# Kernel optimization log

Hardware: AMD Instinct MI355X
Metric: run time of the kernel (lower is better)

The kernel has to match this reference:

```python
import jax, jax.numpy as jnp
import numpy as np

jax.config.update("jax_enable_x64", True)  # packing needs true int64 bit ops

_NORM12 = np.array([
    [3,1,1,1,3,3,3,3],[1,3,1,1,3,3,3,3],[1,1,3,1,3,3,3,3],[1,1,1,3,3,3,3,3],
    [3,3,3,1,3,3,1,1],[3,3,3,1,3,1,3,1],[3,3,3,1,1,3,3,1],[3,3,3,1,3,1,1,3],
    [3,3,3,1,1,3,1,3],[3,3,3,1,1,1,3,3],[3,3,1,3,3,3,1,1],[3,3,1,3,3,1,3,1],
    [3,3,1,3,1,3,3,1],[3,3,1,3,3,1,1,3],[3,3,1,3,1,3,1,3],[3,3,1,3,1,1,3,3],
    [3,1,3,3,3,3,1,1],[3,1,3,3,3,1,3,1],[3,1,3,3,1,3,3,1],[3,1,3,3,3,1,1,3],
    [3,1,3,3,1,3,1,3],[1,3,3,3,1,1,3,3],[1,3,3,3,3,3,1,1],[1,3,3,3,3,1,3,1],
    [1,3,3,3,1,3,3,1],[1,3,3,3,3,1,1,3],[1,3,3,3,1,3,1,3],[1,1,3,3,1,3,3,3],
    [3,3,1,1,3,3,3,1]], dtype=np.float32) / 2.0


def _build_packed_abs_grid():
    # faithful numpy port of get_packed_abs_grid()
    intr = np.arange(-4, 4)
    d8 = np.stack(np.meshgrid(*([intr] * 8), indexing='ij'), axis=-1).reshape(-1, 8).astype(np.float32) + 0.5
    mask = ((d8.sum(-1) % 2) == 0) & ((d8 * d8).sum(-1) <= 10)
    d8abs = np.unique(np.abs(d8[mask]), axis=0)
    cba = np.concatenate([d8abs, _NORM12], axis=0)          # [256, 8]
    cba = cba[:, [0, 2, 4, 6, 1, 3, 5, 7]]
    cba[:, 7] = cba[:, 7] * (1 - 2 * (cba.sum(1) % 2))
    cba = (cba * 2 + 8).astype(np.int64)
    acc = cba[:, 0].copy()
    for i in range(7):
        acc |= cba[:, i + 1] << ((i + 1) * 4)
    return acc                                              # [256] packed nibbles


def _build_full_grid(packed):
    # reconstruct the 2^16-entry E8P grid from the packed abs codewords
    SHUF = np.array([0, 4, 1, 5, 2, 6, 3, 7])               # inverse of [0,2,4,6,1,3,5,7]
    c = np.arange(1 << 16)
    signs = c & 255
    absi = c >> 8
    parity = (((signs[:, None] >> np.arange(8)) & 1).sum(1)) & 1
    signs = signs ^ parity
    nib = ((packed[absi][:, None] >> (4 * SHUF[None, :])) & 15).astype(np.float32)
    val = (nib - 8.0) / 2.0                                 # undo cba*2+8
    sbit = (signs[:, None] >> SHUF[None, :]) & 1
    val = np.where(sbit == 1, -val, val)
    val = val - 0.25 * parity[:, None].astype(np.float32)   # odd-parity coset shift
    return val.astype(np.float32)                           # [65536, 8]


def setup_inputs() -> dict:
    key = jax.random.key(0)
    packed = _build_packed_abs_grid()
    grid = jnp.asarray(_build_full_grid(packed))            # [65536, 8]
    grid_norm = (grid * grid).sum(-1)                       # [65536]
    X = jax.random.normal(key, (256, 32, 8), dtype=jnp.float32)
    return {"X": X, "grid": grid, "grid_norm": grid_norm}


def _pack_idxs(idxs):
    # faithful port of maybe_pack_idxs; idxs: int64 [m, n], m%16==0, n%8==0
    m, n = idxs.shape
    q = idxs.reshape(m // 2, 2, n // 2, 2).transpose(0, 2, 1, 3)   # [m//2, n//2, 2, 2]
    abs32 = ((q[:, :, 0, 0] >> 8)
             + ((q[:, :, 1, 0] >> 8) << 8)
             + ((q[:, :, 0, 1] >> 8) << 16)
             + ((q[:, :, 1, 1] >> 8) << 24))
    sign32 = jnp.zeros_like(abs32)
    for i in range(4):
        wt = q[:, :, i % 2, i // 2]
        for j in range(8):
            sign32 = sign32 + (((wt >> j) & 1) << (4 * j + i))
    out = (sign32 << 32) + abs32
    out = out.reshape(m // 16, 8, n // 8, 4).transpose(0, 2, 1, 3)
    return out.reshape(m, n // 4)


def reference(X, grid, grid_norm):
    m, n, _ = X.shape
    Xf = X.reshape(-1, 8)                                   # [m*n, 8]
    scores = 2.0 * (Xf @ grid.T) - grid_norm                # [m*n, 65536] (traffic-bound)
    idxs = jnp.argmax(scores, axis=-1).astype(jnp.int64)    # [m*n]
    vals = grid[idxs].reshape(m, n, 8)
    idxs = idxs.reshape(m, n)
    packed = _pack_idxs(idxs)                               # [m, n//4] int64
    return vals, idxs, packed
```

## Files before the change

kernel.cpp:

```cpp
#include <hip/hip_runtime.h>
#include <stdint.h>
#include <math.h>


__device__ __forceinline__ void cmp_keep(float& bs, int& bc, float s, int c) {
    if (s > bs || (s == bs && c < bc)) { bs = s; bc = c; }
}

__device__ __forceinline__ double pay_abs(double t, uint32_t pk16) {
    long long ll = __double_as_longlong(t) & 0x7FFFFFFFFFFF0000ll;
    return __longlong_as_double(ll | (long long)pk16);
}

struct TournOut { double a1c, a2c; uint32_t q1, q2; };

__device__ __forceinline__ TournOut tourn8(const double kk[8]) {
    double m01 = fmin(kk[0], kk[1]), x01 = fmax(kk[0], kk[1]);
    double m23 = fmin(kk[2], kk[3]), x23 = fmax(kk[2], kk[3]);
    double m45 = fmin(kk[4], kk[5]), x45 = fmax(kk[4], kk[5]);
    double m67 = fmin(kk[6], kk[7]), x67 = fmax(kk[6], kk[7]);
    double mA = fmin(m01, m23), sA = fmin(fmax(m01, m23), fmin(x01, x23));
    double mB = fmin(m45, m67), sB = fmin(fmax(m45, m67), fmin(x45, x67));
    double m1 = fmin(mA, mB),   m2 = fmin(fmax(mA, mB), fmin(sA, sB));
    long long b1 = __double_as_longlong(m1);
    long long b2 = __double_as_longlong(m2);
    TournOut o;
    o.a1c = __longlong_as_double(b1 & ~0xFFFFll);
    o.a2c = __longlong_as_double(b2 & ~0xFFFFll);
    o.q1 = (uint32_t)b1 & 0xFFFFu;
    o.q2 = (uint32_t)b2 & 0xFFFFu;
    return o;
}

__global__ __launch_bounds__(256, 4) void e8p_fused2(
    const float* __restrict__ X,
    const float* __restrict__ grid,
    const float* __restrict__ grid_norm,
    float* __restrict__ out)
{
    __shared__ float2   sWp[4][256];
    __shared__ uint32_t sPK[4][256];
    __shared__ uint32_t sMeta[256];
    __shared__ float    sSN[256];
    __shared__ int      sC[4][2];

    const int tid = threadIdx.x;
    const int shuf[8] = {0, 4, 1, 5, 2, 6, 3, 7};

    {
        const float4* g4 = reinterpret_cast<const float4*>(grid + (size_t)tid * 2048);
        float4 lo = g4[0], hi = g4[1];
        float w[8] = {lo.x, lo.y, lo.z, lo.w, hi.x, hi.y, hi.z, hi.w};
        float aw[8]; uint32_t pk[8]; uint32_t wsgnshuf = 0;
#pragma unroll
        for (int j = 0; j < 8; ++j) {
            uint32_t sb = __float_as_uint(w[j]) >> 31;
            wsgnshuf |= sb << shuf[j];
            aw[j] = fabsf(w[j]);
            uint32_t tw = (uint32_t)(2.0f * aw[j]);
            pk[j] = (tw << 13) | ((uint32_t)j << 10) | (1u << shuf[j]);
        }
        sWp[0][tid] = make_float2(aw[0], aw[1]);
        sWp[1][tid] = make_float2(aw[2], aw[3]);
        sWp[2][tid] = make_float2(aw[4], aw[5]);
        sWp[3][tid] = make_float2(aw[6], aw[7]);
#pragma unroll
        for (int i = 0; i < 4; ++i) sPK[i][tid] = pk[2 * i] | (pk[2 * i + 1] << 16);
        sMeta[tid] = wsgnshuf | ((uint32_t)(__popc(wsgnshuf) & 1) << 8);
        sSN[tid] = grid_norm[(size_t)tid * 256];
    }
    __syncthreads();

    const int lane = tid & 63, wid = tid >> 6;
    const int A  = blockIdx.x >> 3;
    const int Bh = blockIdx.x & 7;
    const int rbase = (2 * A + (wid & 1)) * 32 + 4 * Bh + 2 * (wid >> 1);

    double   xd[2][8]; double Sx[2];
    uint32_t sp1b[2], sp0sh[2], sp1sh[2], pp0[2], pp1[2];
#pragma unroll
    for (int s = 0; s < 2; ++s) {
        const float* xr = X + (size_t)(rbase + s) * 8;
        double acc = 0.0; uint32_t m1 = 0, m0s = 0, m1s = 0, p0 = 0, p1 = 0;
#pragma unroll
        for (int j = 0; j < 8; ++j) {
            float xf = xr[j]; double d = (double)xf;
            xd[s][j] = d; acc += d;
            uint32_t b0 = (xf < 0.0f) ? 1u : 0u;
            uint32_t b1 = (d < -0.25) ? 1u : 0u;
            m1 |= b1 << j; m0s |= b0 << shuf[j]; m1s |= b1 << shuf[j];
            p0 ^= b0; p1 ^= b1;
        }
        Sx[s] = acc; sp1b[s] = m1; sp0sh[s] = m0s; sp1sh[s] = m1s; pp0[s] = p0; pp1[s] = p1;
    }

    float bestS[2] = {-INFINITY, -INFINITY};
    int   bestC[2] = {0x7fffffff, 0x7fffffff};

#pragma unroll
    for (int k = 0; k < 4; ++k) {
        const int absi = lane + (k << 6);
        float2 w01 = sWp[0][absi], w23 = sWp[1][absi], w45 = sWp[2][absi], w67 = sWp[3][absi];
        float awf[8] = {w01.x, w01.y, w23.x, w23.y, w45.x, w45.y, w67.x, w67.y};
        uint32_t pw0 = sPK[0][absi], pw1 = sPK[1][absi], pw2 = sPK[2][absi], pw3 = sPK[3][absi];
        uint32_t pk16[8] = {pw0 & 0xFFFFu, pw0 >> 16, pw1 & 0xFFFFu, pw1 >> 16,
                            pw2 & 0xFFFFu, pw2 >> 16, pw3 & 0xFFFFu, pw3 >> 16};
        const uint32_t meta = sMeta[absi];
        const float    sN   = sSN[absi];
        const uint32_t wsh = meta & 0xFFu, wpar = (meta >> 8) & 1u;
        double wdA[8];
#pragma unroll
        for (int j = 0; j < 8; ++j) wdA[j] = (double)awf[j];

#pragma unroll
        for (int s = 0; s < 2; ++s) {
            double t0[8], t1[8];
#pragma unroll
            for (int j = 0; j < 8; ++j) {
                t0[j] = wdA[j] * xd[s][j];
                t1[j] = fma(t0[j], 4.0, wdA[j]);
            }
            {
                double Sab = ((fabs(t0[0]) + fabs(t0[1])) + (fabs(t0[2]) + fabs(t0[3])))
                           + ((fabs(t0[4]) + fabs(t0[5])) + (fabs(t0[6]) + fabs(t0[7])));
                double kk[8];
#pragma unroll
                for (int j = 0; j < 8; ++j) kk[j] = pay_abs(t0[j], pk16[j]);
                TournOut o = tourn8(kk);
                uint32_t sb1 = o.q1 & 0xFFu, sb2 = o.q2 & 0xFFu;
                uint32_t par = wpar ^ pp0[s];
                uint32_t seffb = wsh ^ sp0sh[s];
                double dA = par ? o.a1c : 0.0;
                double dB = par ? o.a2c : (o.a1c + o.a2c);
                uint32_t sbA = par ? sb1 : 0u;
                uint32_t sbB = par ? sb2 : (sb1 ^ sb2);
                { float f = (float)(Sab - 2.0 * dA);
                  cmp_keep(bestS[s], bestC[s], 2.0f * f - sN, (absi << 8) | (int)(seffb ^ sbA)); }
                { float f = (float)(Sab - 2.0 * dB);
                  cmp_keep(bestS[s], bestC[s], 2.0f * f - sN, (absi << 8) | (int)(seffb ^ sbB)); }
            }
            {
                double Sab4 = ((fabs(t1[0]) + fabs(t1[1])) + (fabs(t1[2]) + fabs(t1[3])))
                            + ((fabs(t1[4]) + fabs(t1[5])) + (fabs(t1[6]) + fabs(t1[7])));
                double kk[8];
#pragma unroll
                for (int j = 0; j < 8; ++j) kk[j] = pay_abs(t1[j], pk16[j]);
                TournOut o = tourn8(kk);
                uint32_t sb1 = o.q1 & 0xFFu, sb2 = o.q2 & 0xFFu;
                uint32_t par = wpar ^ pp1[s];
                uint32_t seffb = wsh ^ sp1sh[s];
                double dA = par ? o.a1c : 0.0;
                double dB = par ? o.a2c : (o.a1c + o.a2c);
                uint32_t sbA = par ? sb1 : 0u;
                uint32_t sbB = par ? sb2 : (sb1 ^ sb2);
                float W0 = ((((sp1b[s] >> 0) & 1) ? -awf[0] : awf[0]) + (((sp1b[s] >> 1) & 1) ? -awf[1] : awf[1]))
                         + ((((sp1b[s] >> 2) & 1) ? -awf[2] : awf[2]) + (((sp1b[s] >> 3) & 1) ? -awf[3] : awf[3]))
                         + (((((sp1b[s] >> 4) & 1) ? -awf[4] : awf[4]) + (((sp1b[s] >> 5) & 1) ? -awf[5] : awf[5]))
                         +  ((((sp1b[s] >> 6) & 1) ? -awf[6] : awf[6]) + (((sp1b[s] >> 7) & 1) ? -awf[7] : awf[7])));
                uint32_t j1 = (o.q1 >> 10) & 7u, j2 = (o.q2 >> 10) & 7u;
                float w1f = 0.5f * (float)(o.q1 >> 13);
                float w2f = 0.5f * (float)(o.q2 >> 13);
                float sw1 = ((sp1b[s] >> j1) & 1) ? -w1f : w1f;
                float sw2 = ((sp1b[s] >> j2) & 1) ? -w2f : w2f;
                float swA = par ? sw1 : 0.0f;
                float swB = par ? sw2 : (sw1 + sw2);
                {
                    float Wc = W0 - 2.0f * swA;
                    double E = (Sab4 - 2.0 * dA) - ((double)Wc + Sx[s]);
                    float f = (float)(0.25 * E);
                    float gnv = (sN - 0.5f * Wc) + 0.5f;
                    cmp_keep(bestS[s], bestC[s], 2.0f * f - gnv,
                             (absi << 8) | (int)((seffb ^ sbA) ^ 1u));
                }
                {
                    float Wc = W0 - 2.0f * swB;
                    double E = (Sab4 - 2.0 * dB) - ((double)Wc + Sx[s]);
                    float f = (float)(0.25 * E);
                    float gnv = (sN - 0.5f * Wc) + 0.5f;
                    cmp_keep(bestS[s], bestC[s], 2.0f * f - gnv,
                             (absi << 8) | (int)((seffb ^ sbB) ^ 1u));
                }
            }
        }
    }

#pragma unroll
    for (int off = 32; off > 0; off >>= 1) {
        float s0 = __shfl_xor(bestS[0], off); int c0 = __shfl_xor(bestC[0], off);
        float s1 = __shfl_xor(bestS[1], off); int c1 = __shfl_xor(bestC[1], off);
        cmp_keep(bestS[0], bestC[0], s0, c0);
        cmp_keep(bestS[1], bestC[1], s1, c1);
    }

    if (lane < 2) {
        const int s = lane;
        const int c = bestC[s];
        const int row = rbase + s;
        const float4* gg = reinterpret_cast<const float4*>(grid + (size_t)c * 8);
        float4* v4 = reinterpret_cast<float4*>(out + (size_t)row * 8);
        v4[0] = gg[0]; v4[1] = gg[1];
        out[65536 + row] = (float)c;
        sC[wid][s] = c;
    }
    __syncthreads();

    if (tid < 2) {
        const int q = tid;
        const uint32_t e00 = (uint32_t)sC[2 * q + 0][0];
        const uint32_t e10 = (uint32_t)sC[2 * q + 1][0];
        const uint32_t e01 = (uint32_t)sC[2 * q + 0][1];
        const uint32_t e11 = (uint32_t)sC[2 * q + 1][1];
        const uint32_t abs32 = (e00 >> 8) | ((e10 >> 8) << 8)
                             | ((e01 >> 8) << 16) | ((e11 >> 8) << 24);
        const int Bq = 2 * Bh + q;
        const int f = ((A >> 3) << 7) | ((Bq >> 2) << 5) | ((A & 7) << 2) | (Bq & 3);
        out[73728 + f] = (float)(int32_t)abs32;
    }
}

extern "C" void kernel_launch(void* const* d_in, const int* in_sizes, int n_in,
                              void* d_out, int out_size, void* d_ws, size_t ws_size,
                              hipStream_t stream)
{
    const float* X    = (const float*)d_in[0];
    const float* grid = (const float*)d_in[1];
    const float* gn   = (const float*)d_in[2];
    e8p_fused2<<<1024, 256, 0, stream>>>(X, grid, gn, (float*)d_out);
}
```

Measured before the change: 82.87 us.

## Process one row per wavefront and double grid size to 2048 blocks

Each wavefront now handles a single input row instead of two, and the grid grows from 1024 to 2048 blocks. The launch-bounds occupancy hint is dropped and the outer k loop is no longer force-unrolled, which lowers register pressure. The aim is more parallelism and occupancy in exchange for no reuse of LDS codebook reads across two rows. The cost is that every block repeats the shared-memory table setup, so the setup work and grid loads per row double.

Measured after the change: 76.52 us. 7.7% less time.

```diff
diff --git a/kernel.cpp b/kernel.cpp
--- a/kernel.cpp
+++ b/kernel.cpp
@@ -32,7 +32,7 @@
     return o;
 }
 
-__global__ __launch_bounds__(256, 4) void e8p_fused2(
+__global__ __launch_bounds__(256) void e8p_fused3(
     const float* __restrict__ X,
     const float* __restrict__ grid,
     const float* __restrict__ grid_norm,
@@ -42,7 +42,7 @@
     __shared__ uint32_t sPK[4][256];
     __shared__ uint32_t sMeta[256];
     __shared__ float    sSN[256];
-    __shared__ int      sC[4][2];
+    __shared__ int      sC[4];
 
     const int tid = threadIdx.x;
     const int shuf[8] = {0, 4, 1, 5, 2, 6, 3, 7};
@@ -72,32 +72,25 @@
     __syncthreads();
 
     const int lane = tid & 63, wid = tid >> 6;
-    const int A  = blockIdx.x >> 3;
-    const int Bh = blockIdx.x & 7;
-    const int rbase = (2 * A + (wid & 1)) * 32 + 4 * Bh + 2 * (wid >> 1);
-
-    double   xd[2][8]; double Sx[2];
-    uint32_t sp1b[2], sp0sh[2], sp1sh[2], pp0[2], pp1[2];
-#pragma unroll
-    for (int s = 0; s < 2; ++s) {
-        const float* xr = X + (size_t)(rbase + s) * 8;
-        double acc = 0.0; uint32_t m1 = 0, m0s = 0, m1s = 0, p0 = 0, p1 = 0;
-#pragma unroll
-        for (int j = 0; j < 8; ++j) {
-            float xf = xr[j]; double d = (double)xf;
-            xd[s][j] = d; acc += d;
-            uint32_t b0 = (xf < 0.0f) ? 1u : 0u;
-            uint32_t b1 = (d < -0.25) ? 1u : 0u;
-            m1 |= b1 << j; m0s |= b0 << shuf[j]; m1s |= b1 << shuf[j];
-            p0 ^= b0; p1 ^= b1;
-        }
-        Sx[s] = acc; sp1b[s] = m1; sp0sh[s] = m0s; sp1sh[s] = m1s; pp0[s] = p0; pp1[s] = p1;
-    }
-
-    float bestS[2] = {-INFINITY, -INFINITY};
-    int   bestC[2] = {0x7fffffff, 0x7fffffff};
-
-#pragma unroll
+    const int A = blockIdx.x >> 4, B = blockIdx.x & 15;
+    const int row = A * 64 + (wid >> 1) * 32 + B * 2 + (wid & 1);
+
+    const float* xr = X + (size_t)row * 8;
+    double xd[8], Sx = 0.0;
+    uint32_t sp1b = 0, sp0sh = 0, sp1sh = 0, pp0 = 0, pp1 = 0;
+#pragma unroll
+    for (int j = 0; j < 8; ++j) {
+        float xf = xr[j]; double d = (double)xf;
+        xd[j] = d; Sx += d;
+        uint32_t b0 = (xf < 0.0f) ? 1u : 0u;
+        uint32_t b1 = (d < -0.25) ? 1u : 0u;
+        sp1b |= b1 << j;
+        sp0sh |= b0 << shuf[j]; sp1sh |= b1 << shuf[j];
+        pp0 ^= b0; pp1 ^= b1;
+    }
+
+    float bestS = -INFINITY; int bestC = 0x7fffffff;
+
     for (int k = 0; k < 4; ++k) {
         const int absi = lane + (k << 6);
         float2 w01 = sWp[0][absi], w23 = sWp[1][absi], w45 = sWp[2][absi], w67 = sWp[3][absi];
@@ -108,112 +101,99 @@
         const uint32_t meta = sMeta[absi];
         const float    sN   = sSN[absi];
         const uint32_t wsh = meta & 0xFFu, wpar = (meta >> 8) & 1u;
-        double wdA[8];
-#pragma unroll
-        for (int j = 0; j < 8; ++j) wdA[j] = (double)awf[j];
-
-#pragma unroll
-        for (int s = 0; s < 2; ++s) {
-            double t0[8], t1[8];
-#pragma unroll
-            for (int j = 0; j < 8; ++j) {
-                t0[j] = wdA[j] * xd[s][j];
-                t1[j] = fma(t0[j], 4.0, wdA[j]);
+
+        double kk0[8], t1[8];
+#pragma unroll
+        for (int j = 0; j < 8; ++j) {
+            double wd = (double)awf[j];
+            double t0 = wd * xd[j];
+            t1[j]  = fma(t0, 4.0, wd);
+            kk0[j] = pay_abs(t0, pk16[j]);
+        }
+
+        {
+            double Sab = ((fabs(kk0[0]) + fabs(kk0[1])) + (fabs(kk0[2]) + fabs(kk0[3])))
+                       + ((fabs(kk0[4]) + fabs(kk0[5])) + (fabs(kk0[6]) + fabs(kk0[7])));
+            TournOut o = tourn8(kk0);
+            uint32_t sb1 = o.q1 & 0xFFu, sb2 = o.q2 & 0xFFu;
+            uint32_t par = wpar ^ pp0;
+            uint32_t seffb = wsh ^ sp0sh;
+            double dA = par ? o.a1c : 0.0;
+            double dB = par ? o.a2c : (o.a1c + o.a2c);
+            uint32_t sbA = par ? sb1 : 0u;
+            uint32_t sbB = par ? sb2 : (sb1 ^ sb2);
+            { float f = (float)(Sab - 2.0 * dA);
+              cmp_keep(bestS, bestC, 2.0f * f - sN, (absi << 8) | (int)(seffb ^ sbA)); }
+            { float f = (float)(Sab - 2.0 * dB);
+              cmp_keep(bestS, bestC, 2.0f * f - sN, (absi << 8) | (int)(seffb ^ sbB)); }
+        }
+        {
+            double kk1[8];
+#pragma unroll
+            for (int j = 0; j < 8; ++j) kk1[j] = pay_abs(t1[j], pk16[j]);
+            double Sab4 = ((fabs(kk1[0]) + fabs(kk1[1])) + (fabs(kk1[2]) + fabs(kk1[3])))
+                        + ((fabs(kk1[4]) + fabs(kk1[5])) + (fabs(kk1[6]) + fabs(kk1[7])));
+            TournOut o = tourn8(kk1);
+            uint32_t sb1 = o.q1 & 0xFFu, sb2 = o.q2 & 0xFFu;
+            uint32_t par = wpar ^ pp1;
+            uint32_t seffb = wsh ^ sp1sh;
+            double dA = par ? o.a1c : 0.0;
+            double dB = par ? o.a2c : (o.a1c + o.a2c);
+            uint32_t sbA = par ? sb1 : 0u;
+            uint32_t sbB = par ? sb2 : (sb1 ^ sb2);
+            float W0 = ((((sp1b >> 0) & 1) ? -awf[0] : awf[0]) + (((sp1b >> 1) & 1) ? -awf[1] : awf[1]))
+                     + ((((sp1b >> 2) & 1) ? -awf[2] : awf[2]) + (((sp1b >> 3) & 1) ? -awf[3] : awf[3]))
+                     + (((((sp1b >> 4) & 1) ? -awf[4] : awf[4]) + (((sp1b >> 5) & 1) ? -awf[5] : awf[5]))
+                     +  ((((sp1b >> 6) & 1) ? -awf[6] : awf[6]) + (((sp1b >> 7) & 1) ? -awf[7] : awf[7])));
+            uint32_t j1 = (o.q1 >> 10) & 7u, j2 = (o.q2 >> 10) & 7u;
+            float w1f = 0.5f * (float)(o.q1 >> 13);
+            float w2f = 0.5f * (float)(o.q2 >> 13);
+            float sw1 = ((sp1b >> j1) & 1) ? -w1f : w1f;
+            float sw2 = ((sp1b >> j2) & 1) ? -w2f : w2f;
+            float swA = par ? sw1 : 0.0f;
+            float swB = par ? sw2 : (sw1 + sw2);
+            {
+                float Wc = W0 - 2.0f * swA;
+                double E = (Sab4 - 2.0 * dA) - ((double)Wc + Sx);
+                float f = (float)(0.25 * E);
+                float gnv = (sN - 0.5f * Wc) + 0.5f;
+                cmp_keep(bestS, bestC, 2.0f * f - gnv,
+                         (absi << 8) | (int)((seffb ^ sbA) ^ 1u));
             }
             {
-                double Sab = ((fabs(t0[0]) + fabs(t0[1])) + (fabs(t0[2]) + fabs(t0[3])))
-                           + ((fabs(t0[4]) + fabs(t0[5])) + (fabs(t0[6]) + fabs(t0[7])));
-                double kk[8];
-#pragma unroll
-                for (int j = 0; j < 8; ++j) kk[j] = pay_abs(t0[j], pk16[j]);
-                TournOut o = tourn8(kk);
-                uint32_t sb1 = o.q1 & 0xFFu, sb2 = o.q2 & 0xFFu;
-                uint32_t par = wpar ^ pp0[s];
-                uint32_t seffb = wsh ^ sp0sh[s];
-                double dA = par ? o.a1c : 0.0;
-                double dB = par ? o.a2c : (o.a1c + o.a2c);
-                uint32_t sbA = par ? sb1 : 0u;
-                uint32_t sbB = par ? sb2 : (sb1 ^ sb2);
-                { float f = (float)(Sab - 2.0 * dA);
-                  cmp_keep(bestS[s], bestC[s], 2.0f * f - sN, (absi << 8) | (int)(seffb ^ sbA)); }
-                { float f = (float)(Sab - 2.0 * dB);
-                  cmp_keep(bestS[s], bestC[s], 2.0f * f - sN, (absi << 8) | (int)(seffb ^ sbB)); }
+                float Wc = W0 - 2.0f * swB;
+                double E = (Sab4 - 2.0 * dB) - ((double)Wc + Sx);
+                float f = (float)(0.25 * E);
+                float gnv = (sN - 0.5f * Wc) + 0.5f;
+                cmp_keep(bestS, bestC, 2.0f * f - gnv,
+                         (absi << 8) | (int)((seffb ^ sbB) ^ 1u));
             }
-            {
-                double Sab4 = ((fabs(t1[0]) + fabs(t1[1])) + (fabs(t1[2]) + fabs(t1[3])))
-                            + ((fabs(t1[4]) + fabs(t1[5])) + (fabs(t1[6]) + fabs(t1[7])));
-                double kk[8];
-#pragma unroll
-                for (int j = 0; j < 8; ++j) kk[j] = pay_abs(t1[j], pk16[j]);
-                TournOut o = tourn8(kk);
-                uint32_t sb1 = o.q1 & 0xFFu, sb2 = o.q2 & 0xFFu;
-                uint32_t par = wpar ^ pp1[s];
-                uint32_t seffb = wsh ^ sp1sh[s];
-                double dA = par ? o.a1c : 0.0;
-                double dB = par ? o.a2c : (o.a1c + o.a2c);
-                uint32_t sbA = par ? sb1 : 0u;
-                uint32_t sbB = par ? sb2 : (sb1 ^ sb2);
-                float W0 = ((((sp1b[s] >> 0) & 1) ? -awf[0] : awf[0]) + (((sp1b[s] >> 1) & 1) ? -awf[1] : awf[1]))
-                         + ((((sp1b[s] >> 2) & 1) ? -awf[2] : awf[2]) + (((sp1b[s] >> 3) & 1) ? -awf[3] : awf[3]))
-                         + (((((sp1b[s] >> 4) & 1) ? -awf[4] : awf[4]) + (((sp1b[s] >> 5) & 1) ? -awf[5] : awf[5]))
-                         +  ((((sp1b[s] >> 6) & 1) ? -awf[6] : awf[6]) + (((sp1b[s] >> 7) & 1) ? -awf[7] : awf[7])));
-                uint32_t j1 = (o.q1 >> 10) & 7u, j2 = (o.q2 >> 10) & 7u;
-                float w1f = 0.5f * (float)(o.q1 >> 13);
-                float w2f = 0.5f * (float)(o.q2 >> 13);
-                float sw1 = ((sp1b[s] >> j1) & 1) ? -w1f : w1f;
-                float sw2 = ((sp1b[s] >> j2) & 1) ? -w2f : w2f;
-                float swA = par ? sw1 : 0.0f;
-                float swB = par ? sw2 : (sw1 + sw2);
-                {
-                    float Wc = W0 - 2.0f * swA;
-                    double E = (Sab4 - 2.0 * dA) - ((double)Wc + Sx[s]);
-                    float f = (float)(0.25 * E);
-                    float gnv = (sN - 0.5f * Wc) + 0.5f;
-                    cmp_keep(bestS[s], bestC[s], 2.0f * f - gnv,
-                             (absi << 8) | (int)((seffb ^ sbA) ^ 1u));
-                }
-                {
-                    float Wc = W0 - 2.0f * swB;
-                    double E = (Sab4 - 2.0 * dB) - ((double)Wc + Sx[s]);
-                    float f = (float)(0.25 * E);
-                    float gnv = (sN - 0.5f * Wc) + 0.5f;
-                    cmp_keep(bestS[s], bestC[s], 2.0f * f - gnv,
-                             (absi << 8) | (int)((seffb ^ sbB) ^ 1u));
-                }
-            }
         }
     }
 
 #pragma unroll
     for (int off = 32; off > 0; off >>= 1) {
-        float s0 = __shfl_xor(bestS[0], off); int c0 = __shfl_xor(bestC[0], off);
-        float s1 = __shfl_xor(bestS[1], off); int c1 = __shfl_xor(bestC[1], off);
-        cmp_keep(bestS[0], bestC[0], s0, c0);
-        cmp_keep(bestS[1], bestC[1], s1, c1);
-    }
-
-    if (lane < 2) {
-        const int s = lane;
-        const int c = bestC[s];
-        const int row = rbase + s;
+        float s2 = __shfl_xor(bestS, off);
+        int   c2 = __shfl_xor(bestC, off);
+        cmp_keep(bestS, bestC, s2, c2);
+    }
+
+    if (lane == 0) {
+        const int c = bestC;
         const float4* gg = reinterpret_cast<const float4*>(grid + (size_t)c * 8);
         float4* v4 = reinterpret_cast<float4*>(out + (size_t)row * 8);
         v4[0] = gg[0]; v4[1] = gg[1];
         out[65536 + row] = (float)c;
-        sC[wid][s] = c;
+        sC[wid] = c;
     }
     __syncthreads();
 
-    if (tid < 2) {
-        const int q = tid;
-        const uint32_t e00 = (uint32_t)sC[2 * q + 0][0];
-        const uint32_t e10 = (uint32_t)sC[2 * q + 1][0];
-        const uint32_t e01 = (uint32_t)sC[2 * q + 0][1];
-        const uint32_t e11 = (uint32_t)sC[2 * q + 1][1];
+    if (tid == 0) {
+        const uint32_t e00 = (uint32_t)sC[0], e01 = (uint32_t)sC[1];
+        const uint32_t e10 = (uint32_t)sC[2], e11 = (uint32_t)sC[3];
         const uint32_t abs32 = (e00 >> 8) | ((e10 >> 8) << 8)
                              | ((e01 >> 8) << 16) | ((e11 >> 8) << 24);
-        const int Bq = 2 * Bh + q;
-        const int f = ((A >> 3) << 7) | ((Bq >> 2) << 5) | ((A & 7) << 2) | (Bq & 3);
+        const int f = ((A >> 3) << 7) | ((B >> 2) << 5) | ((A & 7) << 2) | (B & 3);
         out[73728 + f] = (float)(int32_t)abs32;
     }
 }
@@ -225,5 +205,5 @@
     const float* X    = (const float*)d_in[0];
     const float* grid = (const float*)d_in[1];
     const float* gn   = (const float*)d_in[2];
-    e8p_fused2<<<1024, 256, 0, stream>>>(X, grid, gn, (float*)d_out);
-}
+    e8p_fused3<<<2048, 256, 0, stream>>>(X, grid, gn, (float*)d_out);
+}
```
